# Optimization experiments

Hardware: AMD Instinct MI355X
Metric: run time of the kernel (lower is better)

## Reference

```python
import jax, jax.numpy as jnp
import numpy as np

N = 163842   # icosahedron level-7 vertices
CH = 64
EPS = 1e-5
SLOPE = 0.2

def _bn_lrelu(x, g, b):
    # BatchNorm1d over vertex dim (training-mode batch stats, biased var) + LeakyReLU(0.2)
    mu = jnp.mean(x, axis=0)
    var = jnp.var(x, axis=0)
    y = (x - mu) * jax.lax.rsqrt(var + EPS) * g + b
    return jnp.where(y > 0, y, SLOPE * y)

def _onering_conv(x, neigh, W, bias):
    # gather 7 one-ring neighbors per vertex, flatten, linear project
    n = x.shape[0]
    feat = x[neigh].reshape(n, -1)          # [N, 7*C]
    return feat @ W + bias                  # [N, out]

def setup_inputs() -> dict:
    key = jax.random.key(0)
    ks = jax.random.split(key, 8)
    d = {
        "x": jax.random.normal(ks[0], (N, CH), jnp.float32),
        "neigh_orders": jax.random.randint(ks[1], (7 * N,), 0, N, jnp.int64),
    }
    for i, k in enumerate([1, 2, 3, 4]):
        cin = CH * k
        d[f"g{k}"] = jnp.ones((cin,), jnp.float32)
        d[f"b{k}"] = jnp.zeros((cin,), jnp.float32)
        d[f"W{k}"] = jax.random.normal(ks[2 + i], (7 * cin, CH), jnp.float32) * (1.0 / np.sqrt(7 * cin))
        d[f"wb{k}"] = jnp.zeros((CH,), jnp.float32)
    return d

def reference(x, neigh_orders, g1, b1, g2, b2, g3, b3, g4, b4,
              W1, wb1, W2, wb2, W3, wb3, W4, wb4):
    x1 = _onering_conv(_bn_lrelu(x, g1, b1), neigh_orders, W1, wb1)
    c2 = jnp.concatenate((x, x1), axis=1)
    x2 = _onering_conv(_bn_lrelu(c2, g2, b2), neigh_orders, W2, wb2)
    c3 = jnp.concatenate((x, x1, x2), axis=1)
    x3 = _onering_conv(_bn_lrelu(c3, g3, b3), neigh_orders, W3, wb3)
    c4 = jnp.concatenate((x, x1, x2, x3), axis=1)
    x4 = _onering_conv(_bn_lrelu(c4, g4, b4), neigh_orders, W4, wb4)
    return x4
```

## Files before the change

### kernel.cpp

```cpp
#include <hip/hip_runtime.h>
#include <stdint.h>

#define NV 163842
#define EPSV 1e-5f

using short8 = __attribute__((ext_vector_type(8))) short;
using f32x4  = __attribute__((ext_vector_type(4))) float;

static __device__ __forceinline__ unsigned short f2bf(float f) {
    union { float f; unsigned int i; } v; v.f = f;
    return (unsigned short)((v.i + 0x7FFFu + ((v.i >> 16) & 1u)) >> 16);
}
static __device__ __forceinline__ void bf2x(unsigned int w, float& a, float& b) {
    union { unsigned int i; float f; } lo, hi;
    lo.i = w << 16; hi.i = w & 0xFFFF0000u;
    a = lo.f; b = hi.f;
}
static __device__ __forceinline__ unsigned int pack2(float a, float b) {
    union { float f; unsigned int i; } ua, ub; ua.f = a; ub.f = b;
    return __builtin_amdgcn_perm(ub.i + 0x8000u, ua.i + 0x8000u, 0x07060302);
}

static __device__ __forceinline__ void gl_lds16(const unsigned short* g, unsigned short* l) {
    __builtin_amdgcn_global_load_lds((__attribute__((address_space(1))) void*)g,
                                     (__attribute__((address_space(3))) void*)l, 16, 0, 0);
}

__global__ __launch_bounds__(256) void k_zero(float* __restrict__ ACC) {
    ACC[threadIdx.x] = 0.f;
    ACC[256 + threadIdx.x] = 0.f;
}

__global__ __launch_bounds__(256) void k_cast(const float* __restrict__ x,
                                              unsigned short* __restrict__ C,
                                              float* __restrict__ ACC) {
    const int t = threadIdx.x;
    const int wv = t >> 6, lane = t & 63;
    const int v = blockIdx.x * 64 + (t >> 2);
    const int c0 = (t & 3) * 16;
    float f[16];
    const bool valid = v < NV;
    if (valid) {
        const float4* p = (const float4*)(x + (size_t)v * 64 + c0);
#pragma unroll
        for (int i = 0; i < 4; ++i) {
            float4 q = p[i];
            f[i * 4 + 0] = q.x; f[i * 4 + 1] = q.y; f[i * 4 + 2] = q.z; f[i * 4 + 3] = q.w;
        }
        unsigned int o[8];
#pragma unroll
        for (int i = 0; i < 8; ++i)
            o[i] = ((unsigned int)f2bf(f[2 * i])) | (((unsigned int)f2bf(f[2 * i + 1])) << 16);
        uint4* dst = (uint4*)(C + (size_t)v * 256 + c0);
        dst[0] = uint4{o[0], o[1], o[2], o[3]};
        dst[1] = uint4{o[4], o[5], o[6], o[7]};
    } else {
#pragma unroll
        for (int i = 0; i < 16; ++i) f[i] = 0.f;
    }
    float s[16], s2[16];
#pragma unroll
    for (int i = 0; i < 16; ++i) { s[i] = f[i]; s2[i] = f[i] * f[i]; }
#pragma unroll
    for (int mask = 4; mask <= 32; mask <<= 1) {
#pragma unroll
        for (int i = 0; i < 16; ++i) {
            s[i]  += __shfl_xor(s[i],  mask);
            s2[i] += __shfl_xor(s2[i], mask);
        }
    }
    __shared__ float red[4 * 128];
    if ((lane >> 2) == 0) {
        int cb = (lane & 3) * 16;
#pragma unroll
        for (int i = 0; i < 16; ++i) {
            red[wv * 128 + cb + i]      = s[i];
            red[wv * 128 + 64 + cb + i] = s2[i];
        }
    }
    __syncthreads();
    if (t < 128) {
        float v4 = red[t] + red[128 + t] + red[256 + t] + red[384 + t];
        int c = t & 63, which = t >> 6;
        atomicAdd(&ACC[which * 256 + c], v4);
    }
}

__global__ __launch_bounds__(256) void k_wt_all(const float* __restrict__ W1,
                                                const float* __restrict__ W2,
                                                const float* __restrict__ W3,
                                                const float* __restrict__ W4,
                                                unsigned short* __restrict__ WT) {
    int j = blockIdx.x * 256 + threadIdx.x;
    if (j >= 286720) return;
    const float* W; int jj, K7;
    if (j < 28672)       { W = W1; jj = j;          K7 = 448;  }
    else if (j < 86016)  { W = W2; jj = j - 28672;  K7 = 896;  }
    else if (j < 172032) { W = W3; jj = j - 86016;  K7 = 1344; }
    else                 { W = W4; jj = j - 172032; K7 = 1792; }
    int n = jj / K7, k = jj - n * K7;
    WT[j] = f2bf(W[(size_t)k * 64 + n]);
}

template<int CIN>
__global__ __launch_bounds__(256) void k_norm(const unsigned short* __restrict__ C,
                                              const float* __restrict__ ACC,
                                              const float* __restrict__ g,
                                              const float* __restrict__ b,
                                              unsigned short* __restrict__ CN) {
    __shared__ float ssc[256], ssh[256];
    const int t = threadIdx.x;
    if (t < CIN) {
        float s = ACC[t], s2 = ACC[256 + t];
        float mu = s * (1.0f / NV);
        float var = fmaf(-mu, mu, s2 * (1.0f / NV));
        float sc = g[t] * rsqrtf(var + EPSV);
        ssc[t] = sc;
        ssh[t] = b[t] - mu * sc;
    }
    __syncthreads();
    constexpr int C8 = CIN / 8;
    const int total = NV * C8;
    for (int idx = blockIdx.x * 256 + t; idx < total; idx += gridDim.x * 256) {
        int v = idx / C8;
        int c8 = idx - v * C8;
        int ch = c8 * 8;
        uint4 u = *(const uint4*)(C + (size_t)v * 256 + ch);
        unsigned int in[4] = {u.x, u.y, u.z, u.w}, o[4];
#pragma unroll
        for (int j = 0; j < 4; ++j) {
            float lo, hi; bf2x(in[j], lo, hi);
            float y0 = fmaf(lo, ssc[ch + 2 * j],     ssh[ch + 2 * j]);
            float y1 = fmaf(hi, ssc[ch + 2 * j + 1], ssh[ch + 2 * j + 1]);
            y0 = y0 > 0.f ? y0 : 0.2f * y0;
            y1 = y1 > 0.f ? y1 : 0.2f * y1;
            o[j] = pack2(y0, y1);
        }
        *(uint4*)(CN + (size_t)v * CIN + ch) = uint4{o[0], o[1], o[2], o[3]};
    }
}

template<int CIN, int GRP, bool FINAL>
__global__ __launch_bounds__(256) void k_gg(const unsigned short* __restrict__ CN,
                                            const int* __restrict__ neigh,
                                            const unsigned short* __restrict__ WT,
                                            const float* __restrict__ wb,
                                            float* __restrict__ ACC,
                                            unsigned short* __restrict__ Cout,
                                            float* __restrict__ Fout) {
    constexpr int KB = CIN / 64;
    constexpr int K7 = 7 * CIN;

    __shared__ int sIdx[896];
    __shared__ unsigned short sA[128 * 64];
    __shared__ unsigned short sW[64 * 64];

    const int t = threadIdx.x;
    const int v0 = blockIdx.x * 128;
    const int wv = t >> 6, lane = t & 63;
    const int m = lane & 15, quad = lane >> 4;
    const int rowin = lane >> 3, slot = lane & 7;
    const int sw = ((slot ^ rowin) * 8);

    for (int q = t; q < 896; q += 256) {
        int gi = v0 * 7 + q;
        sIdx[q] = (gi < NV * 7) ? neigh[gi] : 0;
    }

    f32x4 acc[2][4];
#pragma unroll
    for (int i = 0; i < 2; ++i)
#pragma unroll
        for (int j = 0; j < 4; ++j) acc[i][j] = f32x4{0.f, 0.f, 0.f, 0.f};

    __syncthreads();

    for (int r = 0; r < 7; ++r) {
        const unsigned short* asrc[4];
#pragma unroll
        for (int i = 0; i < 4; ++i) {
            int gidx = sIdx[(wv * 32 + i * 8 + rowin) * 7 + r];
            asrc[i] = CN + (size_t)gidx * CIN + sw;
        }
#pragma unroll
        for (int kb = 0; kb < KB; ++kb) {
            const int c = r * KB + kb;
#pragma unroll
            for (int i = 0; i < 4; ++i)
                gl_lds16(asrc[i] + kb * 64, sA + (wv * 32 + i * 8) * 64);
#pragma unroll
            for (int j = 0; j < 2; ++j) {
                int n = wv * 16 + j * 8 + rowin;
                gl_lds16(WT + (size_t)n * K7 + c * 64 + sw, sW + (wv * 16 + j * 8) * 64);
            }
            __syncthreads();
#pragma unroll
            for (int s = 0; s < 2; ++s) {
                const int sx = ((s * 4 + quad) ^ (m & 7)) * 8;
                short8 af0 = *(const short8*)(sA + (wv * 32 + m) * 64      + sx);
                short8 af1 = *(const short8*)(sA + (wv * 32 + 16 + m) * 64 + sx);
#pragma unroll
                for (int ct = 0; ct < 4; ++ct) {
                    short8 bf = *(const short8*)(sW + (ct * 16 + m) * 64 + sx);
                    acc[0][ct] = __builtin_amdgcn_mfma_f32_16x16x32_bf16(af0, bf, acc[0][ct], 0, 0, 0);
                    acc[1][ct] = __builtin_amdgcn_mfma_f32_16x16x32_bf16(af1, bf, acc[1][ct], 0, 0, 0);
                }
            }
            __syncthreads();
        }
    }

    float bsum[4]  = {0.f, 0.f, 0.f, 0.f};
    float b2sum[4] = {0.f, 0.f, 0.f, 0.f};
#pragma unroll
    for (int mt = 0; mt < 2; ++mt) {
#pragma unroll
        for (int ct = 0; ct < 4; ++ct) {
            int col = ct * 16 + m;
            float bv = wb[col];
#pragma unroll
            for (int j = 0; j < 4; ++j) {
                int vr = v0 + wv * 32 + mt * 16 + quad * 4 + j;
                float val = acc[mt][ct][j] + bv;
                if (vr < NV) {
                    if (FINAL) {
                        Fout[(size_t)vr * 64 + col] = val;
                    } else {
                        Cout[(size_t)vr * 256 + GRP * 64 + col] = f2bf(val);
                        bsum[ct] += val; b2sum[ct] += val * val;
                    }
                }
            }
        }
    }
    if (!FINAL) {
#pragma unroll
        for (int ct = 0; ct < 4; ++ct) {
            bsum[ct]  += __shfl_xor(bsum[ct], 16);
            bsum[ct]  += __shfl_xor(bsum[ct], 32);
            b2sum[ct] += __shfl_xor(b2sum[ct], 16);
            b2sum[ct] += __shfl_xor(b2sum[ct], 32);
        }
        float* red = (float*)sA;
        if (quad == 0) {
#pragma unroll
            for (int ct = 0; ct < 4; ++ct) {
                red[wv * 128 + ct * 16 + m]       = bsum[ct];
                red[512 + wv * 128 + ct * 16 + m] = b2sum[ct];
            }
        }
        __syncthreads();
        if (t < 128) {
            int c = t & 63, which = t >> 6;
            float v = red[which * 512 + c] + red[which * 512 + 128 + c] +
                      red[which * 512 + 256 + c] + red[which * 512 + 384 + c];
            atomicAdd(&ACC[which * 256 + GRP * 64 + c], v);
        }
    }
}

extern "C" void kernel_launch(void* const* d_in, const int* in_sizes, int n_in,
                              void* d_out, int out_size, void* d_ws, size_t ws_size,
                              hipStream_t stream) {
    const float* x     = (const float*)d_in[0];
    const int*   neigh = (const int*)d_in[1];
    const float* G[4]  = {(const float*)d_in[2],  (const float*)d_in[6],
                          (const float*)d_in[10], (const float*)d_in[14]};
    const float* B[4]  = {(const float*)d_in[3],  (const float*)d_in[7],
                          (const float*)d_in[11], (const float*)d_in[15]};
    const float* W[4]  = {(const float*)d_in[4],  (const float*)d_in[8],
                          (const float*)d_in[12], (const float*)d_in[16]};
    const float* WB[4] = {(const float*)d_in[5],  (const float*)d_in[9],
                          (const float*)d_in[13], (const float*)d_in[17]};
    float* out = (float*)d_out;

    char* ws = (char*)d_ws;
    size_t off = 0;
    unsigned short* C  = (unsigned short*)(ws + off); off += (size_t)NV * 256 * 2;
    unsigned short* CN = (unsigned short*)(ws + off); off += (size_t)NV * 256 * 2;
    unsigned short* WT = (unsigned short*)(ws + off); off += (size_t)286720 * 2;
    float* ACC         = (float*)(ws + off);          off += 512 * 4;

    k_zero<<<1, 256, 0, stream>>>(ACC);
    k_cast<<<(NV + 63) / 64, 256, 0, stream>>>(x, C, ACC);
    k_wt_all<<<(286720 + 255) / 256, 256, 0, stream>>>(W[0], W[1], W[2], W[3], WT);

    const int GG = (NV + 127) / 128;
    const int NB = 2048;

    k_norm< 64><<<NB, 256, 0, stream>>>(C, ACC, G[0], B[0], CN);
    k_gg< 64, 1, false><<<GG, 256, 0, stream>>>(CN, neigh, WT,          WB[0], ACC, C, nullptr);
    k_norm<128><<<NB, 256, 0, stream>>>(C, ACC, G[1], B[1], CN);
    k_gg<128, 2, false><<<GG, 256, 0, stream>>>(CN, neigh, WT + 28672,  WB[1], ACC, C, nullptr);
    k_norm<192><<<NB, 256, 0, stream>>>(C, ACC, G[2], B[2], CN);
    k_gg<192, 3, false><<<GG, 256, 0, stream>>>(CN, neigh, WT + 86016,  WB[2], ACC, C, nullptr);
    k_norm<256><<<NB, 256, 0, stream>>>(C, ACC, G[3], B[3], CN);
    k_gg<256, 0, true ><<<GG, 256, 0, stream>>>(CN, neigh, WT + 172032, WB[3], ACC, nullptr, out);
}
```

Measured before the change: 560.4 us.

## Double-buffer gather-GEMM LDS tiles to overlap loads with MFMA

The gather-GEMM main loop now uses two LDS buffers for the activation and weight tiles. The loads for the next K-chunk are issued before the MFMAs on the current chunk run, so one barrier per step replaces two. It also raises wave priority around the MFMA block. This doubles LDS use per block (about 52KB), which may reduce occupancy. Correctness depends on global_load_lds completion being covered by the barrier wait (vmcnt) before each buffer is reused.

Result: no change. 554.6 us (-1.0%).

```diff
diff --git a/kernel.cpp b/kernel.cpp
--- a/kernel.cpp
+++ b/kernel.cpp
@@ -149,11 +149,12 @@
                                             unsigned short* __restrict__ Cout,
                                             float* __restrict__ Fout) {
     constexpr int KB = CIN / 64;
+    constexpr int NC = 7 * KB;
     constexpr int K7 = 7 * CIN;
 
     __shared__ int sIdx[896];
-    __shared__ unsigned short sA[128 * 64];
-    __shared__ unsigned short sW[64 * 64];
+    __shared__ unsigned short sA[2][128 * 64];
+    __shared__ unsigned short sW[2][64 * 64];
 
     const int t = threadIdx.x;
     const int v0 = blockIdx.x * 128;
@@ -175,40 +176,49 @@
 
     __syncthreads();
 
-    for (int r = 0; r < 7; ++r) {
-        const unsigned short* asrc[4];
+    auto issue_stage = [&](int r, int kb, int c, int b) {
 #pragma unroll
         for (int i = 0; i < 4; ++i) {
             int gidx = sIdx[(wv * 32 + i * 8 + rowin) * 7 + r];
-            asrc[i] = CN + (size_t)gidx * CIN + sw;
-        }
-#pragma unroll
-        for (int kb = 0; kb < KB; ++kb) {
-            const int c = r * KB + kb;
-#pragma unroll
-            for (int i = 0; i < 4; ++i)
-                gl_lds16(asrc[i] + kb * 64, sA + (wv * 32 + i * 8) * 64);
-#pragma unroll
-            for (int j = 0; j < 2; ++j) {
-                int n = wv * 16 + j * 8 + rowin;
-                gl_lds16(WT + (size_t)n * K7 + c * 64 + sw, sW + (wv * 16 + j * 8) * 64);
+            gl_lds16(CN + (size_t)gidx * CIN + kb * 64 + sw, &sA[b][(wv * 32 + i * 8) * 64]);
+        }
+#pragma unroll
+        for (int j = 0; j < 2; ++j) {
+            int n = wv * 16 + j * 8 + rowin;
+            gl_lds16(WT + (size_t)n * K7 + c * 64 + sw, &sW[b][(wv * 16 + j * 8) * 64]);
+        }
+    };
+    auto compute = [&](int b) {
+        __builtin_amdgcn_s_setprio(1);
+#pragma unroll
+        for (int s = 0; s < 2; ++s) {
+            const int sx = ((s * 4 + quad) ^ (m & 7)) * 8;
+            short8 af0 = *(const short8*)(&sA[b][(wv * 32 + m) * 64 + sx]);
+            short8 af1 = *(const short8*)(&sA[b][(wv * 32 + 16 + m) * 64 + sx]);
+#pragma unroll
+            for (int ct = 0; ct < 4; ++ct) {
+                short8 bf = *(const short8*)(&sW[b][(ct * 16 + m) * 64 + sx]);
+                acc[0][ct] = __builtin_amdgcn_mfma_f32_16x16x32_bf16(af0, bf, acc[0][ct], 0, 0, 0);
+                acc[1][ct] = __builtin_amdgcn_mfma_f32_16x16x32_bf16(af1, bf, acc[1][ct], 0, 0, 0);
             }
-            __syncthreads();
-#pragma unroll
-            for (int s = 0; s < 2; ++s) {
-                const int sx = ((s * 4 + quad) ^ (m & 7)) * 8;
-                short8 af0 = *(const short8*)(sA + (wv * 32 + m) * 64      + sx);
-                short8 af1 = *(const short8*)(sA + (wv * 32 + 16 + m) * 64 + sx);
-#pragma unroll
-                for (int ct = 0; ct < 4; ++ct) {
-                    short8 bf = *(const short8*)(sW + (ct * 16 + m) * 64 + sx);
-                    acc[0][ct] = __builtin_amdgcn_mfma_f32_16x16x32_bf16(af0, bf, acc[0][ct], 0, 0, 0);
-                    acc[1][ct] = __builtin_amdgcn_mfma_f32_16x16x32_bf16(af1, bf, acc[1][ct], 0, 0, 0);
-                }
-            }
-            __syncthreads();
-        }
-    }
+        }
+        __builtin_amdgcn_s_setprio(0);
+    };
+
+    issue_stage(0, 0, 0, 0);
+    __syncthreads();
+
+    int r = 0, kb = 0, buf = 0;
+    for (int c = 0; c < NC - 1; ++c) {
+        int kb1 = kb + 1, r1 = r;
+        if (kb1 == KB) { kb1 = 0; r1 = r + 1; }
+        issue_stage(r1, kb1, c + 1, buf ^ 1);
+        compute(buf);
+        __syncthreads();
+        r = r1; kb = kb1; buf ^= 1;
+    }
+    compute(buf);
+    __syncthreads();
 
     float bsum[4]  = {0.f, 0.f, 0.f, 0.f};
     float b2sum[4] = {0.f, 0.f, 0.f, 0.f};
@@ -241,7 +251,7 @@
             b2sum[ct] += __shfl_xor(b2sum[ct], 16);
             b2sum[ct] += __shfl_xor(b2sum[ct], 32);
         }
-        float* red = (float*)sA;
+        float* red = (float*)&sA[0][0];
         if (quad == 0) {
 #pragma unroll
             for (int ct = 0; ct < 4; ++ct) {
```

## Load MFMA operands directly from global into registers, drop LDS staging and barriers

Applied to the files above, without the earlier changes.

The gather-GEMM kernel no longer stages gathered neighbor rows and weight tiles through shared memory with global_load_lds and two barriers per k-block. Each lane now loads its own A and B fragments straight from global memory into registers and issues the MFMAs. The MFMA section is also wrapped in s_setprio to raise wave priority. This removes barrier stalls and LDS traffic and frees LDS for occupancy. In exchange, the weight tile is reloaded redundantly by every wave and latency is less hidden, since there is no cooperative staging.

Result: slower. 849.3 us (+51.6%).

```diff
diff --git a/kernel.cpp b/kernel.cpp
--- a/kernel.cpp
+++ b/kernel.cpp
@@ -19,11 +19,6 @@
 static __device__ __forceinline__ unsigned int pack2(float a, float b) {
     union { float f; unsigned int i; } ua, ub; ua.f = a; ub.f = b;
     return __builtin_amdgcn_perm(ub.i + 0x8000u, ua.i + 0x8000u, 0x07060302);
-}
-
-static __device__ __forceinline__ void gl_lds16(const unsigned short* g, unsigned short* l) {
-    __builtin_amdgcn_global_load_lds((__attribute__((address_space(1))) void*)g,
-                                     (__attribute__((address_space(3))) void*)l, 16, 0, 0);
 }
 
 __global__ __launch_bounds__(256) void k_zero(float* __restrict__ ACC) {
@@ -152,15 +147,13 @@
     constexpr int K7 = 7 * CIN;
 
     __shared__ int sIdx[896];
-    __shared__ unsigned short sA[128 * 64];
-    __shared__ unsigned short sW[64 * 64];
+    __shared__ float red[1024];
 
     const int t = threadIdx.x;
     const int v0 = blockIdx.x * 128;
     const int wv = t >> 6, lane = t & 63;
     const int m = lane & 15, quad = lane >> 4;
-    const int rowin = lane >> 3, slot = lane & 7;
-    const int sw = ((slot ^ rowin) * 8);
+    const int koff = quad * 8;
 
     for (int q = t; q < 896; q += 256) {
         int gi = v0 * 7 + q;
@@ -175,38 +168,36 @@
 
     __syncthreads();
 
+    const int row0 = (wv * 32 + m) * 7;
+    const int row1 = (wv * 32 + 16 + m) * 7;
+
     for (int r = 0; r < 7; ++r) {
-        const unsigned short* asrc[4];
-#pragma unroll
-        for (int i = 0; i < 4; ++i) {
-            int gidx = sIdx[(wv * 32 + i * 8 + rowin) * 7 + r];
-            asrc[i] = CN + (size_t)gidx * CIN + sw;
-        }
+        const unsigned short* a0 = CN + (size_t)sIdx[row0 + r] * CIN + koff;
+        const unsigned short* a1 = CN + (size_t)sIdx[row1 + r] * CIN + koff;
 #pragma unroll
         for (int kb = 0; kb < KB; ++kb) {
             const int c = r * KB + kb;
-#pragma unroll
-            for (int i = 0; i < 4; ++i)
-                gl_lds16(asrc[i] + kb * 64, sA + (wv * 32 + i * 8) * 64);
-#pragma unroll
-            for (int j = 0; j < 2; ++j) {
-                int n = wv * 16 + j * 8 + rowin;
-                gl_lds16(WT + (size_t)n * K7 + c * 64 + sw, sW + (wv * 16 + j * 8) * 64);
+            short8 af[2][2];
+            af[0][0] = *(const short8*)(a0 + kb * 64);
+            af[0][1] = *(const short8*)(a0 + kb * 64 + 32);
+            af[1][0] = *(const short8*)(a1 + kb * 64);
+            af[1][1] = *(const short8*)(a1 + kb * 64 + 32);
+            short8 bfr[4][2];
+#pragma unroll
+            for (int ct = 0; ct < 4; ++ct) {
+                const unsigned short* wp = WT + (size_t)(ct * 16 + m) * K7 + c * 64 + koff;
+                bfr[ct][0] = *(const short8*)(wp);
+                bfr[ct][1] = *(const short8*)(wp + 32);
             }
-            __syncthreads();
-#pragma unroll
-            for (int s = 0; s < 2; ++s) {
-                const int sx = ((s * 4 + quad) ^ (m & 7)) * 8;
-                short8 af0 = *(const short8*)(sA + (wv * 32 + m) * 64      + sx);
-                short8 af1 = *(const short8*)(sA + (wv * 32 + 16 + m) * 64 + sx);
+            __builtin_amdgcn_s_setprio(1);
+#pragma unroll
+            for (int s = 0; s < 2; ++s)
 #pragma unroll
                 for (int ct = 0; ct < 4; ++ct) {
-                    short8 bf = *(const short8*)(sW + (ct * 16 + m) * 64 + sx);
-                    acc[0][ct] = __builtin_amdgcn_mfma_f32_16x16x32_bf16(af0, bf, acc[0][ct], 0, 0, 0);
-                    acc[1][ct] = __builtin_amdgcn_mfma_f32_16x16x32_bf16(af1, bf, acc[1][ct], 0, 0, 0);
+                    acc[0][ct] = __builtin_amdgcn_mfma_f32_16x16x32_bf16(af[0][s], bfr[ct][s], acc[0][ct], 0, 0, 0);
+                    acc[1][ct] = __builtin_amdgcn_mfma_f32_16x16x32_bf16(af[1][s], bfr[ct][s], acc[1][ct], 0, 0, 0);
                 }
-            }
-            __syncthreads();
+            __builtin_amdgcn_s_setprio(0);
         }
     }
 
@@ -241,7 +232,6 @@
             b2sum[ct] += __shfl_xor(b2sum[ct], 16);
             b2sum[ct] += __shfl_xor(b2sum[ct], 32);
         }
-        float* red = (float*)sA;
         if (quad == 0) {
 #pragma unroll
             for (int ct = 0; ct < 4; ++ct) {
```
